# Optimization experiments

Measured on AMD Instinct MI355X. Metric: run time of the kernel, lower is better.

## Reference

```python
import jax, jax.numpy as jnp
import numpy as np

TEMPERATURE = 0.07
EPS = 1e-8  # torch cosine_similarity clamps the norm product at eps


def setup_inputs() -> dict:
    key = jax.random.key(0)
    k1, k2 = jax.random.split(key)
    B, D = 8192, 256
    u = jax.random.normal(k1, (B, D), dtype=jnp.float32)
    v = jax.random.normal(k2, (B, D), dtype=jnp.float32)
    return {"u": u, "v": v}


def _cos_sim_matrix(a, b):
    # pairwise cosine similarity: (a . b) / max(|a||b|, eps)
    dots = a @ b.T                                   # [B, B]
    an = jnp.linalg.norm(a, axis=-1)                 # [B]
    bn = jnp.linalg.norm(b, axis=-1)                 # [B]
    denom = jnp.maximum(an[:, None] * bn[None, :], EPS)
    return dots / denom


def reference(u, v):
    B = u.shape[0]
    sim_uv = _cos_sim_matrix(u, v) / TEMPERATURE     # [B, B]
    sim_uu = _cos_sim_matrix(u, u) / TEMPERATURE     # [B, B]
    eye = jnp.eye(B, dtype=bool)
    pos_loss = jnp.diagonal(sim_uv)                  # [B]
    neg_inf = jnp.array(-jnp.inf, dtype=sim_uv.dtype)
    # off-diagonal entries of both matrices, concatenated per row (2B-2 valid each)
    negative_sim = jnp.concatenate(
        [jnp.where(eye, neg_inf, sim_uv), jnp.where(eye, neg_inf, sim_uu)], axis=1
    )                                                # [B, 2B]
    neg_loss = jax.nn.logsumexp(negative_sim, axis=-1)  # [B]
    return (-pos_loss + neg_loss).mean()
```

## Files before the change

kernel.cpp:

```cpp
#include <hip/hip_runtime.h>
#include <hip/hip_bf16.h>
#include <stdint.h>

#define NB 8192
#define ND 256
#define NW 16384
#define BM 128
#define BN 128
#define NSUB 8
#define SUBW 2048
#define NTILES (SUBW / BN)
#define NBLK 512
#define SQRT_L2E_INVT 4.5398164f
#define LN2F 0.69314718056f

typedef float floatx4 __attribute__((ext_vector_type(4)));
typedef int   intx4   __attribute__((ext_vector_type(4)));
typedef int   intx8   __attribute__((ext_vector_type(8)));

__device__ __forceinline__ void gload_lds16(const void* g, void* l) {
    __builtin_amdgcn_global_load_lds(
        (const __attribute__((address_space(1))) unsigned int*)g,
        (__attribute__((address_space(3))) unsigned int*)l,
        16, 0, 0);
}

__global__ __launch_bounds__(512) void prep_kernel(
    const float* __restrict__ u, const float* __restrict__ v,
    unsigned char* __restrict__ W)
{
    const int t    = threadIdx.x;
    const int row  = blockIdx.x * 8 + (t >> 6);
    const int lane = t & 63;
    const float* src = (row < NB) ? (v + (size_t)row * ND)
                                  : (u + (size_t)(row - NB) * ND);
    float4 x = ((const float4*)src)[lane];
    float ss = x.x * x.x + x.y * x.y + x.z * x.z + x.w * x.w;
#pragma unroll
    for (int off = 1; off < 64; off <<= 1) ss += __shfl_xor(ss, off, 64);
    const float sc = rsqrtf(ss) * SQRT_L2E_INVT;
    int p = __builtin_amdgcn_cvt_pk_fp8_f32(x.x * sc, x.y * sc, 0, false);
    p     = __builtin_amdgcn_cvt_pk_fp8_f32(x.z * sc, x.w * sc, p, true);
    ((int*)(W + (size_t)row * ND))[lane] = p;
}

__global__ __launch_bounds__(256, 2) void dcl_main(
    const unsigned char* __restrict__ W,
    float* __restrict__ partial,
    float* __restrict__ pos,
    int* __restrict__ cnt,
    float* __restrict__ out)
{
    const int b  = blockIdx.x;
    const int ss = b & 7;
    const int rt = b >> 3;
    const int rb = rt * BM;

    const unsigned char* A = W + (size_t)NB * ND;

    __shared__ __align__(16) char lds[65536];

    const int tid  = threadIdx.x;
    const int wave = tid >> 6;
    const int lane = tid & 63;
    const int wm   = wave >> 1;
    const int wn   = wave & 1;
    const int quad = lane >> 4;
    const int tcol = lane & 15;

    {
        const int cb0 = ss * SUBW;
#pragma unroll
        for (int i = 0; i < 8; i++) {
            int o = i * 4096 + wave * 1024 + lane * 16;
            int r = o >> 8;
            int c = (o >> 4) & 15;
            int cg = (c ^ (r & 15)) * 16;
            gload_lds16(A + (size_t)(rb + r) * ND + cg,
                        lds + i * 4096 + wave * 1024);
            gload_lds16(W + (size_t)(cb0 + r) * ND + cg,
                        lds + 32768 + i * 4096 + wave * 1024);
        }
    }
    __syncthreads();

    intx8 af[4][2];
#pragma unroll
    for (int mt = 0; mt < 4; mt++) {
        int r = wm * 64 + mt * 16 + tcol;
#pragma unroll
        for (int ks = 0; ks < 2; ks++) {
            int c0 = ks * 8 + quad * 2;
            intx4 lo = *(const intx4*)(lds + r * 256 + ((c0 ^ (r & 15)) << 4));
            intx4 hi = *(const intx4*)(lds + r * 256 + (((c0 + 1) ^ (r & 15)) << 4));
            intx8 f;
            f[0] = lo[0]; f[1] = lo[1]; f[2] = lo[2]; f[3] = lo[3];
            f[4] = hi[0]; f[5] = hi[1]; f[6] = hi[2]; f[7] = hi[3];
            af[mt][ks] = f;
        }
    }
    __syncthreads();

    float rsum[4][4];
#pragma unroll
    for (int mt = 0; mt < 4; mt++)
#pragma unroll
        for (int reg = 0; reg < 4; reg++) rsum[mt][reg] = 0.f;

    for (int ct = 0; ct < NTILES; ct++) {
        char* curB = (ct & 1) ? lds : (lds + 32768);
        if (ct + 1 < NTILES) {
            char* nxt = ((ct + 1) & 1) ? lds : (lds + 32768);
            const int cbn = ss * SUBW + (ct + 1) * BN;
#pragma unroll
            for (int i = 0; i < 8; i++) {
                int o = i * 4096 + wave * 1024 + lane * 16;
                int r = o >> 8;
                int c = (o >> 4) & 15;
                int cg = (c ^ (r & 15)) * 16;
                gload_lds16(W + (size_t)(cbn + r) * ND + cg,
                            nxt + i * 4096 + wave * 1024);
            }
        }
        const int cb = ss * SUBW + ct * BN;

        floatx4 acc[4][4];
#pragma unroll
        for (int mt = 0; mt < 4; mt++)
#pragma unroll
            for (int nt = 0; nt < 4; nt++) acc[mt][nt] = (floatx4){0.f, 0.f, 0.f, 0.f};

#pragma unroll
        for (int ks = 0; ks < 2; ks++) {
            intx8 bfr[4];
#pragma unroll
            for (int nt = 0; nt < 4; nt++) {
                int r = wn * 64 + nt * 16 + tcol;
                int c0 = ks * 8 + quad * 2;
                intx4 lo = *(const intx4*)(curB + r * 256 + ((c0 ^ (r & 15)) << 4));
                intx4 hi = *(const intx4*)(curB + r * 256 + (((c0 + 1) ^ (r & 15)) << 4));
                intx8 f;
                f[0] = lo[0]; f[1] = lo[1]; f[2] = lo[2]; f[3] = lo[3];
                f[4] = hi[0]; f[5] = hi[1]; f[6] = hi[2]; f[7] = hi[3];
                bfr[nt] = f;
            }
#pragma unroll
            for (int mt = 0; mt < 4; mt++)
#pragma unroll
                for (int nt = 0; nt < 4; nt++)
                    acc[mt][nt] = __builtin_amdgcn_mfma_scale_f32_16x16x128_f8f6f4(
                        af[mt][ks], bfr[nt], acc[mt][nt],
                        0, 0,
                        0, 127,
                        0, 127);
        }

        if (cb != rb && cb != rb + NB) {
#pragma unroll
            for (int mt = 0; mt < 4; mt++)
#pragma unroll
                for (int nt = 0; nt < 4; nt++)
#pragma unroll
                    for (int reg = 0; reg < 4; reg++)
                        rsum[mt][reg] += __builtin_amdgcn_exp2f(acc[mt][nt][reg]);
        } else {
            const bool isuv = (cb == rb);
#pragma unroll
            for (int mt = 0; mt < 4; mt++)
#pragma unroll
                for (int nt = 0; nt < 4; nt++) {
                    const int gcol = cb + wn * 64 + nt * 16 + tcol;
#pragma unroll
                    for (int reg = 0; reg < 4; reg++) {
                        const int grow = rb + wm * 64 + mt * 16 + quad * 4 + reg;
                        float sc = acc[mt][nt][reg];
                        bool diag = (gcol == grow + (isuv ? 0 : NB));
                        if (isuv && diag) pos[grow] = sc;
                        rsum[mt][reg] += diag ? 0.f : __builtin_amdgcn_exp2f(sc);
                    }
                }
        }
        __syncthreads();
    }

#pragma unroll
    for (int mt = 0; mt < 4; mt++)
#pragma unroll
        for (int reg = 0; reg < 4; reg++) {
            float vsum = rsum[mt][reg];
            vsum += __shfl_xor(vsum, 1, 64);
            vsum += __shfl_xor(vsum, 2, 64);
            vsum += __shfl_xor(vsum, 4, 64);
            vsum += __shfl_xor(vsum, 8, 64);
            if (tcol == 0) {
                int lrow = wm * 64 + mt * 16 + quad * 4 + reg;
                ((float*)lds)[wn * 128 + lrow] = vsum;
            }
        }
    __syncthreads();
    if (tid < BM) {
        const float* lf = (const float*)lds;
        partial[(size_t)ss * NB + rb + tid] = lf[tid] + lf[128 + tid];
    }

    __threadfence();
    __shared__ int amlast;
    if (tid == 0) amlast = (atomicAdd(cnt, 1) == NBLK - 1);
    __syncthreads();
    if (!amlast) return;
    __threadfence();

    float s = 0.f;
    for (int i = tid; i < NB; i += 256) {
        float tot = 0.f;
#pragma unroll
        for (int j = 0; j < 8; j++) tot += partial[(size_t)j * NB + i];
        s += logf(tot) - pos[i] * LN2F;
    }
#pragma unroll
    for (int off = 1; off < 64; off <<= 1) s += __shfl_xor(s, off, 64);
    __syncthreads();
    if (lane == 0) ((float*)lds)[wave] = s;
    __syncthreads();
    if (tid == 0) {
        const float* lf = (const float*)lds;
        out[0] = (lf[0] + lf[1] + lf[2] + lf[3]) / (float)NB;
    }
}

extern "C" void kernel_launch(void* const* d_in, const int* in_sizes, int n_in,
                              void* d_out, int out_size, void* d_ws, size_t ws_size,
                              hipStream_t stream) {
    const float* u = (const float*)d_in[0];
    const float* v = (const float*)d_in[1];
    float* out = (float*)d_out;

    char* ws = (char*)d_ws;
    unsigned char* W = (unsigned char*)ws;
    float* partial = (float*)(ws + (size_t)NW * ND);
    float* pos     = partial + NSUB * NB;
    int*   cnt     = (int*)(pos + NB);

    hipMemsetAsync(cnt, 0, sizeof(int), stream);
    prep_kernel<<<NW / 8, 512, 0, stream>>>(u, v, W);
    dcl_main<<<NBLK, 256, 0, stream>>>(W, partial, pos, cnt, out);
}
```

Before: 150.1 us.

## Use 512-thread blocks with 4 column strips and fold counter reset into prep

The main kernel now runs 256 blocks of 512 threads. Eight waves tile a 128x128 output tile as 2x4, and each block covers a 4096-wide column strip instead of 2048, with separate LDS regions for A and double-buffered B (96KB). The counter reset moves from a memset into the prep kernel, which removes one launch. Each wave does fewer MFMAs per tile and the per-block loop is longer, but there are only 256 blocks on a 256-CU part, and the larger LDS footprint may limit occupancy to one block per CU.

Result: faster. 138.7 us (-7.6%).

```diff
diff --git a/kernel.cpp b/kernel.cpp
--- a/kernel.cpp
+++ b/kernel.cpp
@@ -7,10 +7,10 @@
 #define NW 16384
 #define BM 128
 #define BN 128
-#define NSUB 8
-#define SUBW 2048
-#define NTILES (SUBW / BN)
-#define NBLK 512
+#define NSTRIP 4
+#define STRIPW 4096
+#define NTILES (STRIPW / BN)
+#define NBLK 256
 #define SQRT_L2E_INVT 4.5398164f
 #define LN2F 0.69314718056f
 
@@ -27,8 +27,9 @@
 
 __global__ __launch_bounds__(512) void prep_kernel(
     const float* __restrict__ u, const float* __restrict__ v,
-    unsigned char* __restrict__ W)
+    unsigned char* __restrict__ W, int* __restrict__ cnt)
 {
+    if (blockIdx.x == 0 && threadIdx.x == 0) *cnt = 0;
     const int t    = threadIdx.x;
     const int row  = blockIdx.x * 8 + (t >> 6);
     const int lane = t & 63;
@@ -44,7 +45,7 @@
     ((int*)(W + (size_t)row * ND))[lane] = p;
 }
 
-__global__ __launch_bounds__(256, 2) void dcl_main(
+__global__ __launch_bounds__(512, 2) void dcl_main(
     const unsigned char* __restrict__ W,
     float* __restrict__ partial,
     float* __restrict__ pos,
@@ -52,34 +53,34 @@
     float* __restrict__ out)
 {
     const int b  = blockIdx.x;
-    const int ss = b & 7;
-    const int rt = b >> 3;
+    const int s  = (b >> 1) & 3;
+    const int rt = ((b >> 3) << 1) | (b & 1);
     const int rb = rt * BM;
 
     const unsigned char* A = W + (size_t)NB * ND;
 
-    __shared__ __align__(16) char lds[65536];
+    __shared__ __align__(16) char lds[98304];
 
     const int tid  = threadIdx.x;
     const int wave = tid >> 6;
     const int lane = tid & 63;
-    const int wm   = wave >> 1;
-    const int wn   = wave & 1;
+    const int wm   = wave >> 2;
+    const int wn   = wave & 3;
     const int quad = lane >> 4;
     const int tcol = lane & 15;
 
     {
-        const int cb0 = ss * SUBW;
-#pragma unroll
-        for (int i = 0; i < 8; i++) {
-            int o = i * 4096 + wave * 1024 + lane * 16;
+        const int cb0 = s * STRIPW;
+#pragma unroll
+        for (int i = 0; i < 4; i++) {
+            int o = i * 8192 + wave * 1024 + lane * 16;
             int r = o >> 8;
             int c = (o >> 4) & 15;
             int cg = (c ^ (r & 15)) * 16;
             gload_lds16(A + (size_t)(rb + r) * ND + cg,
-                        lds + i * 4096 + wave * 1024);
+                        lds + i * 8192 + wave * 1024);
             gload_lds16(W + (size_t)(cb0 + r) * ND + cg,
-                        lds + 32768 + i * 4096 + wave * 1024);
+                        lds + 32768 + i * 8192 + wave * 1024);
         }
     }
     __syncthreads();
@@ -99,7 +100,6 @@
             af[mt][ks] = f;
         }
     }
-    __syncthreads();
 
     float rsum[4][4];
 #pragma unroll
@@ -108,58 +108,61 @@
         for (int reg = 0; reg < 4; reg++) rsum[mt][reg] = 0.f;
 
     for (int ct = 0; ct < NTILES; ct++) {
-        char* curB = (ct & 1) ? lds : (lds + 32768);
+        char* curB = lds + 32768 + (ct & 1) * 32768;
         if (ct + 1 < NTILES) {
-            char* nxt = ((ct + 1) & 1) ? lds : (lds + 32768);
-            const int cbn = ss * SUBW + (ct + 1) * BN;
-#pragma unroll
-            for (int i = 0; i < 8; i++) {
-                int o = i * 4096 + wave * 1024 + lane * 16;
+            char* nxt = lds + 32768 + ((ct + 1) & 1) * 32768;
+            const int cbn = s * STRIPW + (ct + 1) * BN;
+#pragma unroll
+            for (int i = 0; i < 4; i++) {
+                int o = i * 8192 + wave * 1024 + lane * 16;
                 int r = o >> 8;
                 int c = (o >> 4) & 15;
                 int cg = (c ^ (r & 15)) * 16;
                 gload_lds16(W + (size_t)(cbn + r) * ND + cg,
-                            nxt + i * 4096 + wave * 1024);
+                            nxt + i * 8192 + wave * 1024);
             }
         }
-        const int cb = ss * SUBW + ct * BN;
-
-        floatx4 acc[4][4];
-#pragma unroll
-        for (int mt = 0; mt < 4; mt++)
-#pragma unroll
-            for (int nt = 0; nt < 4; nt++) acc[mt][nt] = (floatx4){0.f, 0.f, 0.f, 0.f};
-
-#pragma unroll
-        for (int ks = 0; ks < 2; ks++) {
-            intx8 bfr[4];
-#pragma unroll
-            for (int nt = 0; nt < 4; nt++) {
-                int r = wn * 64 + nt * 16 + tcol;
+        const int cb = s * STRIPW + ct * BN;
+
+        intx8 bfr[2][2];
+#pragma unroll
+        for (int nt = 0; nt < 2; nt++) {
+            int r = wn * 32 + nt * 16 + tcol;
+#pragma unroll
+            for (int ks = 0; ks < 2; ks++) {
                 int c0 = ks * 8 + quad * 2;
                 intx4 lo = *(const intx4*)(curB + r * 256 + ((c0 ^ (r & 15)) << 4));
                 intx4 hi = *(const intx4*)(curB + r * 256 + (((c0 + 1) ^ (r & 15)) << 4));
                 intx8 f;
                 f[0] = lo[0]; f[1] = lo[1]; f[2] = lo[2]; f[3] = lo[3];
                 f[4] = hi[0]; f[5] = hi[1]; f[6] = hi[2]; f[7] = hi[3];
-                bfr[nt] = f;
+                bfr[nt][ks] = f;
             }
+        }
+
+        floatx4 acc[4][2];
+#pragma unroll
+        for (int mt = 0; mt < 4; mt++)
+#pragma unroll
+            for (int nt = 0; nt < 2; nt++) acc[mt][nt] = (floatx4){0.f, 0.f, 0.f, 0.f};
+
+#pragma unroll
+        for (int ks = 0; ks < 2; ks++)
 #pragma unroll
             for (int mt = 0; mt < 4; mt++)
 #pragma unroll
-                for (int nt = 0; nt < 4; nt++)
+                for (int nt = 0; nt < 2; nt++)
                     acc[mt][nt] = __builtin_amdgcn_mfma_scale_f32_16x16x128_f8f6f4(
-                        af[mt][ks], bfr[nt], acc[mt][nt],
+                        af[mt][ks], bfr[nt][ks], acc[mt][nt],
                         0, 0,
                         0, 127,
                         0, 127);
-        }
 
         if (cb != rb && cb != rb + NB) {
 #pragma unroll
             for (int mt = 0; mt < 4; mt++)
 #pragma unroll
-                for (int nt = 0; nt < 4; nt++)
+                for (int nt = 0; nt < 2; nt++)
 #pragma unroll
                     for (int reg = 0; reg < 4; reg++)
                         rsum[mt][reg] += __builtin_amdgcn_exp2f(acc[mt][nt][reg]);
@@ -168,8 +171,8 @@
 #pragma unroll
             for (int mt = 0; mt < 4; mt++)
 #pragma unroll
-                for (int nt = 0; nt < 4; nt++) {
-                    const int gcol = cb + wn * 64 + nt * 16 + tcol;
+                for (int nt = 0; nt < 2; nt++) {
+                    const int gcol = cb + wn * 32 + nt * 16 + tcol;
 #pragma unroll
                     for (int reg = 0; reg < 4; reg++) {
                         const int grow = rb + wm * 64 + mt * 16 + quad * 4 + reg;
@@ -200,31 +203,35 @@
     __syncthreads();
     if (tid < BM) {
         const float* lf = (const float*)lds;
-        partial[(size_t)ss * NB + rb + tid] = lf[tid] + lf[128 + tid];
+        partial[(size_t)s * NB + rb + tid] =
+            lf[tid] + lf[128 + tid] + lf[256 + tid] + lf[384 + tid];
     }
 
     __threadfence();
+    __syncthreads();
     __shared__ int amlast;
     if (tid == 0) amlast = (atomicAdd(cnt, 1) == NBLK - 1);
     __syncthreads();
     if (!amlast) return;
     __threadfence();
 
-    float s = 0.f;
-    for (int i = tid; i < NB; i += 256) {
-        float tot = 0.f;
-#pragma unroll
-        for (int j = 0; j < 8; j++) tot += partial[(size_t)j * NB + i];
-        s += logf(tot) - pos[i] * LN2F;
-    }
-#pragma unroll
-    for (int off = 1; off < 64; off <<= 1) s += __shfl_xor(s, off, 64);
-    __syncthreads();
-    if (lane == 0) ((float*)lds)[wave] = s;
+    float sacc = 0.f;
+    for (int i = tid; i < NB; i += 512) {
+        float tot = partial[i] + partial[NB + i] + partial[2 * NB + i]
+                  + partial[3 * NB + i];
+        sacc += logf(tot) - pos[i] * LN2F;
+    }
+#pragma unroll
+    for (int off = 1; off < 64; off <<= 1) sacc += __shfl_xor(sacc, off, 64);
+    __syncthreads();
+    if (lane == 0) ((float*)lds)[wave] = sacc;
     __syncthreads();
     if (tid == 0) {
         const float* lf = (const float*)lds;
-        out[0] = (lf[0] + lf[1] + lf[2] + lf[3]) / (float)NB;
+        float tot = 0.f;
+#pragma unroll
+        for (int i = 0; i < 8; i++) tot += lf[i];
+        out[0] = tot / (float)NB;
     }
 }
 
@@ -238,10 +245,9 @@
     char* ws = (char*)d_ws;
     unsigned char* W = (unsigned char*)ws;
     float* partial = (float*)(ws + (size_t)NW * ND);
-    float* pos     = partial + NSUB * NB;
+    float* pos     = partial + NSTRIP * NB;
     int*   cnt     = (int*)(pos + NB);
 
-    hipMemsetAsync(cnt, 0, sizeof(int), stream);
-    prep_kernel<<<NW / 8, 512, 0, stream>>>(u, v, W);
-    dcl_main<<<NBLK, 256, 0, stream>>>(W, partial, pos, cnt, out);
-}
+    prep_kernel<<<NW / 8, 512, 0, stream>>>(u, v, W, cnt);
+    dcl_main<<<NBLK, 512, 0, stream>>>(W, partial, pos, cnt, out);
+}
```
